# Kernel tuning notes

Measured on AMD Instinct MI355X. Metric: run time of the kernel, lower is better.

Reference implementation:

```python
import jax, jax.numpy as jnp
import numpy as np

C1 = 512
RATIO = 16


def setup_inputs() -> dict:
    key = jax.random.key(0)
    k1, k2, k3 = jax.random.split(key, 3)
    x = jax.random.normal(k1, (32, C1, 64, 64), dtype=jnp.float32)
    # Linear(c1, c1//ratio, bias=False): weight shape (out, in)
    w1 = jax.random.normal(k2, (C1 // RATIO, C1), dtype=jnp.float32) * (1.0 / np.sqrt(C1))
    w2 = jax.random.normal(k3, (C1, C1 // RATIO), dtype=jnp.float32) * (1.0 / np.sqrt(C1 // RATIO))
    return {"x": x, "w1": w1, "w2": w2}


def reference(x, w1, w2):
    b, c, h, w = x.shape
    # squeeze: global avg pool -> (b, c)
    y = jnp.mean(x, axis=(2, 3))
    # excitation MLP: Linear -> ReLU -> Linear -> Sigmoid
    y = jax.nn.relu(jnp.einsum('bc,rc->br', y, w1))
    y = jax.nn.sigmoid(jnp.einsum('br,cr->bc', y, w2))
    # top half channels by gate value (torch.sort descending + slice == top_k)
    half_ch = c // 2
    y_half, indices = jax.lax.top_k(y, half_ch)  # (b, half_ch)
    # per-sample channel gather, then scale by the gate
    x_half = jnp.take_along_axis(x, indices[:, :, None, None], axis=1)  # (b, half_ch, h, w)
    return x_half * y_half[:, :, None, None]
```

## Files before the change

### kernel.cpp

```cpp
#include <hip/hip_runtime.h>
#include <math.h>

#define B    32
#define C    512
#define R    32
#define HW   4096
#define HALF 256

typedef float v4f __attribute__((ext_vector_type(4)));

__global__ __launch_bounds__(256) void se_mean_kernel(const float* __restrict__ x,
                                                      float* __restrict__ means) {
    const int t    = threadIdx.x;
    const int lane = t & 63;
    const int wid  = t >> 6;
    const int row0 = (blockIdx.x * 4 + wid) * 2;
    const v4f* p0 = (const v4f*)(x + (size_t)row0 * HW);
    const v4f* p1 = (const v4f*)(x + (size_t)row0 * HW + HW);

    v4f va[16], vb[16];
#pragma unroll
    for (int i = 0; i < 16; ++i) va[i] = p0[lane + 64 * i];
#pragma unroll
    for (int i = 0; i < 16; ++i) vb[i] = p1[lane + 64 * i];

    float s0 = 0.f, s1 = 0.f;
#pragma unroll
    for (int i = 0; i < 16; ++i) s0 += (va[i].x + va[i].y) + (va[i].z + va[i].w);
#pragma unroll
    for (int i = 0; i < 16; ++i) s1 += (vb[i].x + vb[i].y) + (vb[i].z + vb[i].w);

#pragma unroll
    for (int off = 32; off > 0; off >>= 1) {
        s0 += __shfl_down(s0, off, 64);
        s1 += __shfl_down(s1, off, 64);
    }
    if (lane == 0) {
        means[row0]     = s0 * (1.0f / HW);
        means[row0 + 1] = s1 * (1.0f / HW);
    }
}

__global__ __launch_bounds__(512) void se_gate_topk_kernel(const float* __restrict__ means,
                                                           const float* __restrict__ w1,
                                                           const float* __restrict__ w2,
                                                           int* __restrict__ idx_out,
                                                           float* __restrict__ gate_out) {
    const int b = blockIdx.x;
    const int t = threadIdx.x;
    __shared__ float sm[C];
    __shared__ float ps[R][17];
    __shared__ float sy1[R];
    __shared__ float sy2[C];

    sm[t] = means[b * C + t];
    __syncthreads();

    {
        const int r   = t & 31;
        const int seg = t >> 5;
        const int c0  = seg * 32;
        float acc = 0.f;
#pragma unroll
        for (int i = 0; i < 32; ++i) acc += sm[c0 + i] * w1[r * C + c0 + i];
        ps[r][seg] = acc;
    }
    __syncthreads();
    if (t < R) {
        float acc = 0.f;
#pragma unroll
        for (int s = 0; s < 16; ++s) acc += ps[t][s];
        sy1[t] = fmaxf(acc, 0.f);
    }
    __syncthreads();

    {
        float acc = 0.f;
#pragma unroll
        for (int r = 0; r < R; ++r) acc += sy1[r] * w2[t * R + r];
        sy2[t] = 1.0f / (1.0f + expf(-acc));
    }
    __syncthreads();

    const float v = sy2[t];
    const v4f* sv = (const v4f*)sy2;
    int rank = 0;
#pragma unroll 4
    for (int j4 = 0; j4 < C / 4; ++j4) {
        v4f u = sv[j4];
        const int j = j4 * 4;
        rank += (u.x > v) || (u.x == v && (j + 0) < t);
        rank += (u.y > v) || (u.y == v && (j + 1) < t);
        rank += (u.z > v) || (u.z == v && (j + 2) < t);
        rank += (u.w > v) || (u.w == v && (j + 3) < t);
    }
    if (rank < HALF) {
        idx_out[b * HALF + rank]  = t;
        gate_out[b * HALF + rank] = v;
    }
}

__global__ __launch_bounds__(256) void se_gather_scale_kernel(const float* __restrict__ x,
                                                              const int* __restrict__ idx,
                                                              const float* __restrict__ gate,
                                                              float* __restrict__ out) {
    const int t    = threadIdx.x;
    const int lane = t & 63;
    const int wid  = t >> 6;
    const int bk   = blockIdx.x * 4 + wid;
    const int b    = bk >> 8;
    const int ch   = idx[bk];
    const float g  = gate[bk];
    const v4f* src = (const v4f*)(x + ((size_t)b * C + ch) * HW);
    v4f* dst = (v4f*)(out + (size_t)bk * HW);

#pragma unroll
    for (int i = 0; i < 16; ++i) {
        v4f v = src[lane + 64 * i];
        v *= g;
        __builtin_nontemporal_store(v, &dst[lane + 64 * i]);
    }
}

extern "C" void kernel_launch(void* const* d_in, const int* in_sizes, int n_in,
                              void* d_out, int out_size, void* d_ws, size_t ws_size,
                              hipStream_t stream) {
    const float* x  = (const float*)d_in[0];
    const float* w1 = (const float*)d_in[1];
    const float* w2 = (const float*)d_in[2];
    float* out = (float*)d_out;

    float* means = (float*)d_ws;
    int*   idx   = (int*)((char*)d_ws + B * C * 4);
    float* gate  = (float*)((char*)d_ws + B * C * 4 + B * HALF * 4);

    se_mean_kernel<<<B * C / 8, 256, 0, stream>>>(x, means);
    se_gate_topk_kernel<<<B, 512, 0, stream>>>(means, w1, w2, idx, gate);
    se_gather_scale_kernel<<<B * HALF / 4, 256, 0, stream>>>(x, idx, gate, out);
}
```

Measured before the change: 429.8 us.

## Fuse mean, gate/top-k and gather into one cooperative persistent kernel

Replaces the three separate launches with a single cooperative kernel that uses grid-wide syncs between the mean-reduction, MLP gate/top-k, and gather-scale phases, with persistent waves striding over rows. This removes two kernel launch boundaries and their tail gaps. The cost is two grid.sync barriers, a gate phase that runs on only 32 blocks while the rest wait, and lower memory-level parallelism per wave than the old two-row mean kernel. The old three-kernel path stays as a fallback if the cooperative launch fails.

```diff
diff --git a/kernel.cpp b/kernel.cpp
--- a/kernel.cpp
+++ b/kernel.cpp
@@ -1,13 +1,123 @@
 #include <hip/hip_runtime.h>
+#include <hip/hip_cooperative_groups.h>
 #include <math.h>
+
+namespace cg = cooperative_groups;
 
 #define B    32
 #define C    512
 #define R    32
 #define HW   4096
 #define HALF 256
+#define TPB  256
 
 typedef float v4f __attribute__((ext_vector_type(4)));
+
+__global__ __launch_bounds__(TPB, 4) void se_fused_kernel(const float* __restrict__ x,
+                                                          const float* __restrict__ w1,
+                                                          const float* __restrict__ w2,
+                                                          float* __restrict__ means,
+                                                          int* __restrict__ idx,
+                                                          float* __restrict__ gate,
+                                                          float* __restrict__ out) {
+    cg::grid_group grid = cg::this_grid();
+    const int t      = threadIdx.x;
+    const int lane   = t & 63;
+    const int wid    = t >> 6;
+    const int nwaves = gridDim.x * 4;
+    const int gw     = blockIdx.x * 4 + wid;
+
+    for (int row = gw; row < B * C; row += nwaves) {
+        const v4f* p = (const v4f*)(x + (size_t)row * HW);
+        v4f v[16];
+#pragma unroll
+        for (int i = 0; i < 16; ++i) v[i] = p[lane + 64 * i];
+        float s = 0.f;
+#pragma unroll
+        for (int i = 0; i < 16; ++i) s += (v[i].x + v[i].y) + (v[i].z + v[i].w);
+#pragma unroll
+        for (int off = 32; off > 0; off >>= 1) s += __shfl_down(s, off, 64);
+        if (lane == 0) means[row] = s * (1.0f / HW);
+    }
+
+    grid.sync();
+
+    __shared__ float sm[C];
+    __shared__ float ps[R][9];
+    __shared__ float sy1[R];
+    __shared__ float sy2[C];
+    for (int b = blockIdx.x; b < B; b += gridDim.x) {
+        sm[t]       = means[b * C + t];
+        sm[t + 256] = means[b * C + t + 256];
+        __syncthreads();
+
+        {
+            const int r   = t & 31;
+            const int seg = t >> 5;
+            const int c0  = seg * 64;
+            float acc = 0.f;
+#pragma unroll
+            for (int i = 0; i < 64; ++i) acc += sm[c0 + i] * w1[r * C + c0 + i];
+            ps[r][seg] = acc;
+        }
+        __syncthreads();
+        if (t < R) {
+            float acc = 0.f;
+#pragma unroll
+            for (int s = 0; s < 8; ++s) acc += ps[t][s];
+            sy1[t] = fmaxf(acc, 0.f);
+        }
+        __syncthreads();
+
+#pragma unroll
+        for (int h = 0; h < 2; ++h) {
+            const int c = t + h * 256;
+            float acc = 0.f;
+#pragma unroll
+            for (int r = 0; r < R; ++r) acc += sy1[r] * w2[c * R + r];
+            sy2[c] = 1.0f / (1.0f + expf(-acc));
+        }
+        __syncthreads();
+
+#pragma unroll
+        for (int h = 0; h < 2; ++h) {
+            const int c = t + h * 256;
+            const float v = sy2[c];
+            const v4f* sv = (const v4f*)sy2;
+            int rank = 0;
+#pragma unroll 4
+            for (int j4 = 0; j4 < C / 4; ++j4) {
+                v4f u = sv[j4];
+                const int j = j4 * 4;
+                rank += (u.x > v) || (u.x == v && (j + 0) < c);
+                rank += (u.y > v) || (u.y == v && (j + 1) < c);
+                rank += (u.z > v) || (u.z == v && (j + 2) < c);
+                rank += (u.w > v) || (u.w == v && (j + 3) < c);
+            }
+            if (rank < HALF) {
+                idx[b * HALF + rank]  = c;
+                gate[b * HALF + rank] = v;
+            }
+        }
+        __syncthreads();
+    }
+
+    grid.sync();
+
+    for (int bk = gw; bk < B * HALF; bk += nwaves) {
+        const int b   = bk >> 8;
+        const int ch  = idx[bk];
+        const float g = gate[bk];
+        const v4f* src = (const v4f*)(x + ((size_t)b * C + ch) * HW);
+        v4f* dst = (v4f*)(out + (size_t)bk * HW);
+#pragma unroll
+        for (int i = 0; i < 16; ++i) {
+            v4f v = src[lane + 64 * i];
+            v *= g;
+            __builtin_nontemporal_store(v, &dst[lane + 64 * i]);
+        }
+    }
+}
 
 __global__ __launch_bounds__(256) void se_mean_kernel(const float* __restrict__ x,
                                                       float* __restrict__ means) {
@@ -55,7 +165,6 @@
 
     sm[t] = means[b * C + t];
     __syncthreads();
-
     {
         const int r   = t & 31;
         const int seg = t >> 5;
@@ -73,7 +182,6 @@
         sy1[t] = fmaxf(acc, 0.f);
     }
     __syncthreads();
-
     {
         float acc = 0.f;
 #pragma unroll
@@ -134,7 +242,31 @@
     int*   idx   = (int*)((char*)d_ws + B * C * 4);
     float* gate  = (float*)((char*)d_ws + B * C * 4 + B * HALF * 4);
 
-    se_mean_kernel<<<B * C / 8, 256, 0, stream>>>(x, means);
-    se_gate_topk_kernel<<<B, 512, 0, stream>>>(means, w1, w2, idx, gate);
-    se_gather_scale_kernel<<<B * HALF / 4, 256, 0, stream>>>(x, idx, gate, out);
-}
+    static int coop_grid = -2;
+    if (coop_grid == -2) {
+        int maxB = 0, cus = 0, dev = 0;
+        (void)hipGetDevice(&dev);
+        if (hipOccupancyMaxActiveBlocksPerMultiprocessor(&maxB, (const void*)se_fused_kernel,
+                                                         TPB, 0) != hipSuccess) maxB = 0;
+        if (hipDeviceGetAttribute(&cus, hipDeviceAttributeMultiprocessorCount, dev) != hipSuccess) cus = 0;
+        long total = (long)maxB * (long)cus;
+        coop_grid = (total >= 64) ? (int)(total > 2048 ? 2048 : total) : -1;
+    }
+
+    bool done = false;
+    if (coop_grid > 0) {
+        void* args[] = {(void*)&x, (void*)&w1, (void*)&w2,
+                        (void*)&means, (void*)&idx, (void*)&gate, (void*)&out};
+        if (hipLaunchCooperativeKernel((const void*)se_fused_kernel, dim3(coop_grid), dim3(TPB),
+                                       args, 0, stream) == hipSuccess) {
+            done = true;
+        } else {
+            coop_grid = -1;
+        }
+    }
+    if (!done) {
+        se_mean_kernel<<<B * C / 8, 256, 0, stream>>>(x, means);
+        se_gate_topk_kernel<<<B, 512, 0, stream>>>(means, w1, w2, idx, gate);
+        se_gather_scale_kernel<<<B * HALF / 4, 256, 0, stream>>>(x, idx, gate, out);
+    }
+}
```

After: 576.8 us. +34.2%, slower.
